# Performance work log

Measured on AMD Instinct MI355X. Metric: run time of the kernel, lower is better.

Reference implementation:

```python
import jax, jax.numpy as jnp
import numpy as np

TOPK = 4          # config.top_prob_values
NBINS = 32        # config.max_num_bins -> bins per corner = NBINS+1 = 33
HID = 64          # config.lqe_hidden_dim
B, L = 64, 4096


def setup_inputs() -> dict:
    key = jax.random.key(0)
    k1, k2, k3, k4 = jax.random.split(key, 4)
    in_dim = 4 * (TOPK + 1)  # 20
    scores = jax.random.normal(k1, (B, L, 1), dtype=jnp.float32)
    pred_corners = jax.random.normal(k2, (B, L, 4 * (NBINS + 1)), dtype=jnp.float32)
    # Deimv2MLP (DFineMLP) with num_layers=2: Linear(20,64) -> relu -> Linear(64,1)
    w1 = jax.random.normal(k3, (in_dim, HID), dtype=jnp.float32) / np.sqrt(in_dim)
    b1 = jnp.zeros((HID,), dtype=jnp.float32)
    w2 = jax.random.normal(k4, (HID, 1), dtype=jnp.float32) / np.sqrt(HID)
    b2 = jnp.zeros((1,), dtype=jnp.float32)
    return {"scores": scores, "pred_corners": pred_corners,
            "w1": w1, "b1": b1, "w2": w2, "b2": b2}


def reference(scores, pred_corners, w1, b1, w2, b2):
    b, l, _ = pred_corners.shape
    # softmax over bins per corner: (B, L, 4, NBINS+1)
    prob = jax.nn.softmax(pred_corners.reshape(b, l, 4, NBINS + 1), axis=-1)
    prob_topk, _ = jax.lax.top_k(prob, TOPK)                     # (B, L, 4, TOPK)
    stat = jnp.concatenate([prob_topk,
                            prob_topk.mean(axis=-1, keepdims=True)], axis=-1)
    stat = stat.reshape(b, l, 4 * (TOPK + 1))                    # (B, L, 20)
    h = jax.nn.relu(stat @ w1 + b1)                              # (B, L, 64)
    quality_score = h @ w2 + b2                                  # (B, L, 1)
    return scores + quality_score
```

## Files before the change

### kernel.cpp

```cpp
#include <hip/hip_runtime.h>


#define THREADS 256
#define ROWS 64

typedef float f32x4 __attribute__((ext_vector_type(4), aligned(16)));

__device__ __forceinline__ void sort4d(float& a, float& b, float& c, float& d) {
    float t;
    t = fmaxf(a, b); b = fminf(a, b); a = t;
    t = fmaxf(c, d); d = fminf(c, d); c = t;
    t = fmaxf(a, c); c = fminf(a, c); a = t;
    t = fmaxf(b, d); d = fminf(b, d); b = t;
    t = fmaxf(b, c); c = fminf(b, c); b = t;
}
__device__ __forceinline__ void ins4(float& a, float& b, float& c, float& d,
                                     float x) {
    float t;
    t = fmaxf(a, x); x = fminf(a, x); a = t;
    t = fmaxf(b, x); x = fminf(b, x); b = t;
    t = fmaxf(c, x); x = fminf(c, x); c = t;
    d = fmaxf(d, x);
}
__device__ __forceinline__ void merge4(float& a0, float& a1, float& a2,
                                       float& a3, float b0, float b1,
                                       float b2, float b3) {
    a0 = fmaxf(a0, b3);
    a1 = fmaxf(a1, b2);
    a2 = fmaxf(a2, b1);
    a3 = fmaxf(a3, b0);
    sort4d(a0, a1, a2, a3);
}

__global__ __launch_bounds__(THREADS, 4)
void lqe_kernel(const float* __restrict__ scores,
                const float* __restrict__ pc,
                const float* __restrict__ w1,
                const float* __restrict__ b1,
                const float* __restrict__ w2,
                const float* __restrict__ b2,
                float* __restrict__ out)
{
    __shared__ float sm_stage[ROWS * 132];
    __shared__ float sm_stat[ROWS * 21];

    const int t = threadIdx.x;
    const long long rowBase = (long long)blockIdx.x * ROWS;

    {
        const f32x4* __restrict__ src = (const f32x4*)(pc + rowBase * 132);
        f32x4* dst = (f32x4*)sm_stage;
        #pragma unroll
        for (int i = 0; i < 8; ++i) dst[t + i * 256] = src[t + i * 256];
        if (t < 64) dst[2048 + t] = src[2048 + t];
    }
    __syncthreads();

    {
        const float* v = sm_stage + t * 33;
        float x[33];
        #pragma unroll
        for (int k = 0; k < 33; ++k) x[k] = v[k];

        float a0 = x[0],  a1 = x[1],  a2 = x[2],  a3 = x[3];
        float c0 = x[8],  c1 = x[9],  c2 = x[10], c3 = x[11];
        float d0 = x[16], d1 = x[17], d2 = x[18], d3 = x[19];
        float e0 = x[24], e1 = x[25], e2 = x[26], e3 = x[27];
        sort4d(a0, a1, a2, a3);
        sort4d(c0, c1, c2, c3);
        sort4d(d0, d1, d2, d3);
        sort4d(e0, e1, e2, e3);
        #pragma unroll
        for (int k = 0; k < 4; ++k) {
            ins4(a0, a1, a2, a3, x[4 + k]);
            ins4(c0, c1, c2, c3, x[12 + k]);
            ins4(d0, d1, d2, d3, x[20 + k]);
            ins4(e0, e1, e2, e3, x[28 + k]);
        }
        ins4(e0, e1, e2, e3, x[32]);
        merge4(a0, a1, a2, a3, c0, c1, c2, c3);
        merge4(d0, d1, d2, d3, e0, e1, e2, e3);
        merge4(a0, a1, a2, a3, d0, d1, d2, d3);
        const float t0 = a0, t1 = a1, t2 = a2, t3 = a3;

        float sa = 0.f, sb = 0.f, sc = 0.f, sd = 0.f;
        #pragma unroll
        for (int k = 0; k < 32; k += 4) {
            sa += __expf(x[k + 0] - t0);
            sb += __expf(x[k + 1] - t0);
            sc += __expf(x[k + 2] - t0);
            sd += __expf(x[k + 3] - t0);
        }
        sa += __expf(x[32] - t0);
        const float inv = 1.0f / ((sa + sb) + (sc + sd));
        const float p0 = inv;
        const float p1 = __expf(t1 - t0) * inv;
        const float p2 = __expf(t2 - t0) * inv;
        const float p3 = __expf(t3 - t0) * inv;
        const float pm = 0.25f * (p0 + p1 + p2 + p3);

        float* sd_ = sm_stat + (t >> 2) * 21 + (t & 3) * 5;
        sd_[0] = p0; sd_[1] = p1; sd_[2] = p2; sd_[3] = p3; sd_[4] = pm;
    }
    __syncthreads();

    {
        const int l  = t & 63;
        const int wv = __builtin_amdgcn_readfirstlane(t >> 6);
        const float* __restrict__ w1s = w1 + wv * 16;
        const float* __restrict__ w2s = w2 + wv * 16;
        const float* __restrict__ b1s = b1 + wv * 16;

        float st[20];
        #pragma unroll
        for (int k = 0; k < 20; ++k) st[k] = sm_stat[l * 21 + k];

        float h[16];
        #pragma unroll
        for (int j = 0; j < 16; ++j) h[j] = b1s[j];
        #pragma unroll
        for (int k = 0; k < 20; ++k) {
            #pragma unroll
            for (int j = 0; j < 16; ++j)
                h[j] = fmaf(st[k], w1s[k * 64 + j], h[j]);
        }
        float acc0 = 0.f, acc1 = 0.f, acc2 = 0.f, acc3 = 0.f;
        #pragma unroll
        for (int j = 0; j < 16; j += 4) {
            acc0 = fmaf(fmaxf(h[j + 0], 0.f), w2s[j + 0], acc0);
            acc1 = fmaf(fmaxf(h[j + 1], 0.f), w2s[j + 1], acc1);
            acc2 = fmaf(fmaxf(h[j + 2], 0.f), w2s[j + 2], acc2);
            acc3 = fmaf(fmaxf(h[j + 3], 0.f), w2s[j + 3], acc3);
        }
        sm_stage[wv * 64 + l] = (acc0 + acc1) + (acc2 + acc3);
    }
    __syncthreads();

    if (t < 64) {
        const float r = (sm_stage[t] + sm_stage[64 + t]) +
                        (sm_stage[128 + t] + sm_stage[192 + t]);
        out[rowBase + t] = scores[rowBase + t] + r + b2[0];
    }
}

extern "C" void kernel_launch(void* const* d_in, const int* in_sizes, int n_in,
                              void* d_out, int out_size, void* d_ws, size_t ws_size,
                              hipStream_t stream) {
    const float* scores = (const float*)d_in[0];
    const float* pc     = (const float*)d_in[1];
    const float* w1     = (const float*)d_in[2];
    const float* b1     = (const float*)d_in[3];
    const float* w2     = (const float*)d_in[4];
    const float* b2     = (const float*)d_in[5];
    float* out = (float*)d_out;

    const int rows = out_size;
    const int blocks = rows / ROWS;
    lqe_kernel<<<blocks, THREADS, 0, stream>>>(scores, pc, w1, b1, w2, b2, out);
}
```

Before: 32.66 us.

## Double-buffer row groups with async global-to-LDS loads across persistent blocks

Each block now handles eight groups of 64 rows instead of one. Two LDS buffers alternate: the next group is prefetched with global_load_lds (direct global-to-LDS DMA) while the current group's softmax, top-k and MLP run. The aim is to hide load latency behind compute and cut per-block launch and staging overhead. The cost is about double the LDS per block and launch bounds lowered to 2 blocks per CU, so fewer loads are in flight per CU, which may hurt a kernel that is limited by memory bandwidth.

```diff
diff --git a/kernel.cpp b/kernel.cpp
--- a/kernel.cpp
+++ b/kernel.cpp
@@ -2,9 +2,18 @@
 
 
 #define THREADS 256
-#define ROWS 64
+#define GROUPS 8
+#define GROUP_ROWS 64
 
 typedef float f32x4 __attribute__((ext_vector_type(4), aligned(16)));
+
+#define BAR_LGKM() asm volatile("s_waitcnt lgkmcnt(0)\n\ts_barrier" ::: "memory")
+
+__device__ __forceinline__ void gll16(const float* g, float* l) {
+    __builtin_amdgcn_global_load_lds(
+        (const __attribute__((address_space(1))) void*)g,
+        (__attribute__((address_space(3))) void*)l, 16, 0, 0);
+}
 
 __device__ __forceinline__ void sort4d(float& a, float& b, float& c, float& d) {
     float t;
@@ -32,7 +41,7 @@
     sort4d(a0, a1, a2, a3);
 }
 
-__global__ __launch_bounds__(THREADS, 4)
+__global__ __launch_bounds__(THREADS, 2)
 void lqe_kernel(const float* __restrict__ scores,
                 const float* __restrict__ pc,
                 const float* __restrict__ w1,
@@ -41,23 +50,28 @@
                 const float* __restrict__ b2,
                 float* __restrict__ out)
 {
-    __shared__ float sm_stage[ROWS * 132];
-    __shared__ float sm_stat[ROWS * 21];
+    __shared__ float smA[GROUP_ROWS * 132];
+    __shared__ float smB[GROUP_ROWS * 132];
+    __shared__ float smStat[GROUP_ROWS * 21];
 
     const int t = threadIdx.x;
-    const long long rowBase = (long long)blockIdx.x * ROWS;
-
-    {
-        const f32x4* __restrict__ src = (const f32x4*)(pc + rowBase * 132);
-        f32x4* dst = (f32x4*)sm_stage;
-        #pragma unroll
-        for (int i = 0; i < 8; ++i) dst[t + i * 256] = src[t + i * 256];
-        if (t < 64) dst[2048 + t] = src[2048 + t];
-    }
-    __syncthreads();
-
-    {
-        const float* v = sm_stage + t * 33;
+    const int l = t & 63;
+    const long long blockRow0 = (long long)blockIdx.x * (GROUPS * GROUP_ROWS);
+    const float b2v = b2[0];
+
+    auto stage_async = [&](int g, float* buf) {
+        const float* src = pc + (blockRow0 + (long long)g * GROUP_ROWS) * 132;
+        const int wvOff = __builtin_amdgcn_readfirstlane(t >> 6) * 64;
+        #pragma unroll
+        for (int i = 0; i < 8; ++i)
+            gll16(src + (size_t)(i * 256 + wvOff + l) * 4,
+                  buf + (size_t)(i * 256 + wvOff) * 4);
+        if (t < 64)
+            gll16(src + (size_t)(2048 + l) * 4, buf + (size_t)2048 * 4);
+    };
+
+    auto corner = [&](const float* buf) {
+        const float* v = buf + t * 33;
         float x[33];
         #pragma unroll
         for (int k = 0; k < 33; ++k) x[k] = v[k];
@@ -99,13 +113,11 @@
         const float p3 = __expf(t3 - t0) * inv;
         const float pm = 0.25f * (p0 + p1 + p2 + p3);
 
-        float* sd_ = sm_stat + (t >> 2) * 21 + (t & 3) * 5;
+        float* sd_ = smStat + (t >> 2) * 21 + (t & 3) * 5;
         sd_[0] = p0; sd_[1] = p1; sd_[2] = p2; sd_[3] = p3; sd_[4] = pm;
-    }
-    __syncthreads();
-
-    {
-        const int l  = t & 63;
+    };
+
+    auto mlp = [&](float* buf) {
         const int wv = __builtin_amdgcn_readfirstlane(t >> 6);
         const float* __restrict__ w1s = w1 + wv * 16;
         const float* __restrict__ w2s = w2 + wv * 16;
@@ -113,7 +125,7 @@
 
         float st[20];
         #pragma unroll
-        for (int k = 0; k < 20; ++k) st[k] = sm_stat[l * 21 + k];
+        for (int k = 0; k < 20; ++k) st[k] = smStat[l * 21 + k];
 
         float h[16];
         #pragma unroll
@@ -132,14 +144,42 @@
             acc2 = fmaf(fmaxf(h[j + 2], 0.f), w2s[j + 2], acc2);
             acc3 = fmaf(fmaxf(h[j + 3], 0.f), w2s[j + 3], acc3);
         }
-        sm_stage[wv * 64 + l] = (acc0 + acc1) + (acc2 + acc3);
-    }
+        buf[wv * 64 + l] = (acc0 + acc1) + (acc2 + acc3);
+    };
+
+    stage_async(0, smA);
     __syncthreads();
 
-    if (t < 64) {
-        const float r = (sm_stage[t] + sm_stage[64 + t]) +
-                        (sm_stage[128 + t] + sm_stage[192 + t]);
-        out[rowBase + t] = scores[rowBase + t] + r + b2[0];
+    #pragma unroll 1
+    for (int gp = 0; gp < GROUPS; gp += 2) {
+        {
+            float sc0 = 0.f;
+            if (t < 64) sc0 = scores[blockRow0 + (long long)gp * 64 + t];
+            if (gp + 1 < GROUPS) stage_async(gp + 1, smB);
+            corner(smA);
+            BAR_LGKM();
+            mlp(smA);
+            BAR_LGKM();
+            if (t < 64)
+                out[blockRow0 + (long long)gp * 64 + t] =
+                    sc0 + (smA[t] + smA[64 + t]) + (smA[128 + t] + smA[192 + t]) + b2v;
+            asm volatile("s_waitcnt vmcnt(0)" ::: "memory");
+            __syncthreads();
+        }
+        {
+            float sc1 = 0.f;
+            if (t < 64) sc1 = scores[blockRow0 + (long long)(gp + 1) * 64 + t];
+            if (gp + 2 < GROUPS) stage_async(gp + 2, smA);
+            corner(smB);
+            BAR_LGKM();
+            mlp(smB);
+            BAR_LGKM();
+            if (t < 64)
+                out[blockRow0 + (long long)(gp + 1) * 64 + t] =
+                    sc1 + (smB[t] + smB[64 + t]) + (smB[128 + t] + smB[192 + t]) + b2v;
+            asm volatile("s_waitcnt vmcnt(0)" ::: "memory");
+            __syncthreads();
+        }
     }
 }
 
@@ -155,6 +195,6 @@
     float* out = (float*)d_out;
 
     const int rows = out_size;
-    const int blocks = rows / ROWS;
+    const int blocks = rows / (GROUPS * GROUP_ROWS);
     lqe_kernel<<<blocks, THREADS, 0, stream>>>(scores, pc, w1, b1, w2, b2, out);
 }
```

Result: slower. 37.89 us (+16.0%).

## Process two row tiles per block with register-prefetched second tile

Applied to the files above, without the earlier changes.

Each block now handles 128 rows instead of 64. Both 64-row tiles of pred_corners (and the scores) are loaded into registers up front, so the second tile's global load overlaps the first tile's softmax/top-k and MLP. The plain __syncthreads are replaced with an inline s_waitcnt lgkmcnt(0) + s_barrier, which avoids waiting on outstanding global loads at each barrier. The cost is roughly 64 extra VGPRs for the buffered tile and half as many blocks, which may lower occupancy for a kernel that is mostly bandwidth-bound.

```diff
diff --git a/kernel.cpp b/kernel.cpp
--- a/kernel.cpp
+++ b/kernel.cpp
@@ -2,9 +2,10 @@
 
 
 #define THREADS 256
-#define ROWS 64
 
 typedef float f32x4 __attribute__((ext_vector_type(4), aligned(16)));
+
+#define BAR_LGKM() asm volatile("s_waitcnt lgkmcnt(0)\n\ts_barrier" ::: "memory")
 
 __device__ __forceinline__ void sort4d(float& a, float& b, float& c, float& d) {
     float t;
@@ -30,6 +31,89 @@
     a2 = fmaxf(a2, b1);
     a3 = fmaxf(a3, b0);
     sort4d(a0, a1, a2, a3);
+}
+
+__device__ __forceinline__ void corner_phase(const float* __restrict__ stage,
+                                             float* __restrict__ stat, int t) {
+    const float* v = stage + t * 33;
+    float x[33];
+    #pragma unroll
+    for (int k = 0; k < 33; ++k) x[k] = v[k];
+
+    float a0 = x[0],  a1 = x[1],  a2 = x[2],  a3 = x[3];
+    float c0 = x[8],  c1 = x[9],  c2 = x[10], c3 = x[11];
+    float d0 = x[16], d1 = x[17], d2 = x[18], d3 = x[19];
+    float e0 = x[24], e1 = x[25], e2 = x[26], e3 = x[27];
+    sort4d(a0, a1, a2, a3);
+    sort4d(c0, c1, c2, c3);
+    sort4d(d0, d1, d2, d3);
+    sort4d(e0, e1, e2, e3);
+    #pragma unroll
+    for (int k = 0; k < 4; ++k) {
+        ins4(a0, a1, a2, a3, x[4 + k]);
+        ins4(c0, c1, c2, c3, x[12 + k]);
+        ins4(d0, d1, d2, d3, x[20 + k]);
+        ins4(e0, e1, e2, e3, x[28 + k]);
+    }
+    ins4(e0, e1, e2, e3, x[32]);
+    merge4(a0, a1, a2, a3, c0, c1, c2, c3);
+    merge4(d0, d1, d2, d3, e0, e1, e2, e3);
+    merge4(a0, a1, a2, a3, d0, d1, d2, d3);
+    const float t0 = a0, t1 = a1, t2 = a2, t3 = a3;
+
+    float sa = 0.f, sb = 0.f, sc = 0.f, sd = 0.f;
+    #pragma unroll
+    for (int k = 0; k < 32; k += 4) {
+        sa += __expf(x[k + 0] - t0);
+        sb += __expf(x[k + 1] - t0);
+        sc += __expf(x[k + 2] - t0);
+        sd += __expf(x[k + 3] - t0);
+    }
+    sa += __expf(x[32] - t0);
+    const float inv = 1.0f / ((sa + sb) + (sc + sd));
+    const float p0 = inv;
+    const float p1 = __expf(t1 - t0) * inv;
+    const float p2 = __expf(t2 - t0) * inv;
+    const float p3 = __expf(t3 - t0) * inv;
+    const float pm = 0.25f * (p0 + p1 + p2 + p3);
+
+    float* sd_ = stat + (t >> 2) * 21 + (t & 3) * 5;
+    sd_[0] = p0; sd_[1] = p1; sd_[2] = p2; sd_[3] = p3; sd_[4] = pm;
+}
+
+__device__ __forceinline__ void mlp_phase(const float* __restrict__ stat,
+                                          float* __restrict__ part, int t,
+                                          const float* __restrict__ w1,
+                                          const float* __restrict__ b1,
+                                          const float* __restrict__ w2) {
+    const int l  = t & 63;
+    const int wv = __builtin_amdgcn_readfirstlane(t >> 6);
+    const float* __restrict__ w1s = w1 + wv * 16;
+    const float* __restrict__ w2s = w2 + wv * 16;
+    const float* __restrict__ b1s = b1 + wv * 16;
+
+    float st[20];
+    #pragma unroll
+    for (int k = 0; k < 20; ++k) st[k] = stat[l * 21 + k];
+
+    float h[16];
+    #pragma unroll
+    for (int j = 0; j < 16; ++j) h[j] = b1s[j];
+    #pragma unroll
+    for (int k = 0; k < 20; ++k) {
+        #pragma unroll
+        for (int j = 0; j < 16; ++j)
+            h[j] = fmaf(st[k], w1s[k * 64 + j], h[j]);
+    }
+    float acc0 = 0.f, acc1 = 0.f, acc2 = 0.f, acc3 = 0.f;
+    #pragma unroll
+    for (int j = 0; j < 16; j += 4) {
+        acc0 = fmaf(fmaxf(h[j + 0], 0.f), w2s[j + 0], acc0);
+        acc1 = fmaf(fmaxf(h[j + 1], 0.f), w2s[j + 1], acc1);
+        acc2 = fmaf(fmaxf(h[j + 2], 0.f), w2s[j + 2], acc2);
+        acc3 = fmaf(fmaxf(h[j + 3], 0.f), w2s[j + 3], acc3);
+    }
+    part[wv * 64 + l] = (acc0 + acc1) + (acc2 + acc3);
 }
 
 __global__ __launch_bounds__(THREADS, 4)
@@ -41,106 +125,64 @@
                 const float* __restrict__ b2,
                 float* __restrict__ out)
 {
-    __shared__ float sm_stage[ROWS * 132];
-    __shared__ float sm_stat[ROWS * 21];
+    __shared__ float smStage[64 * 132];
+    __shared__ float smStat[64 * 21];
+    __shared__ float smPart[256];
 
     const int t = threadIdx.x;
-    const long long rowBase = (long long)blockIdx.x * ROWS;
+    const long long rowBase = (long long)blockIdx.x * 128;
+    const float b2v = b2[0];
+
+    float sc0 = 0.f, sc1 = 0.f;
+    if (t < 64) {
+        sc0 = scores[rowBase + t];
+        sc1 = scores[rowBase + 64 + t];
+    }
+
+    const f32x4* __restrict__ s0 = (const f32x4*)(pc + rowBase * 132);
+    const f32x4* __restrict__ s1 = (const f32x4*)(pc + (rowBase + 64) * 132);
+    f32x4 ra[8], rb[8], taA = {0,0,0,0}, tbB = {0,0,0,0};
+    #pragma unroll
+    for (int i = 0; i < 8; ++i) ra[i] = s0[t + i * 256];
+    if (t < 64) taA = s0[2048 + t];
+    #pragma unroll
+    for (int i = 0; i < 8; ++i) rb[i] = s1[t + i * 256];
+    if (t < 64) tbB = s1[2048 + t];
+    __builtin_amdgcn_sched_barrier(0);
 
     {
-        const f32x4* __restrict__ src = (const f32x4*)(pc + rowBase * 132);
-        f32x4* dst = (f32x4*)sm_stage;
+        f32x4* dst = (f32x4*)smStage;
         #pragma unroll
-        for (int i = 0; i < 8; ++i) dst[t + i * 256] = src[t + i * 256];
-        if (t < 64) dst[2048 + t] = src[2048 + t];
-    }
-    __syncthreads();
+        for (int i = 0; i < 8; ++i) dst[t + i * 256] = ra[i];
+        if (t < 64) dst[2048 + t] = taA;
+    }
+    BAR_LGKM();
+
+    corner_phase(smStage, smStat, t);
+    BAR_LGKM();
+    mlp_phase(smStat, smPart, t, w1, b1, w2);
+    BAR_LGKM();
+    if (t < 64)
+        out[rowBase + t] =
+            sc0 + (smPart[t] + smPart[64 + t]) +
+                  (smPart[128 + t] + smPart[192 + t]) + b2v;
 
     {
-        const float* v = sm_stage + t * 33;
-        float x[33];
+        f32x4* dst = (f32x4*)smStage;
         #pragma unroll
-        for (int k = 0; k < 33; ++k) x[k] = v[k];
-
-        float a0 = x[0],  a1 = x[1],  a2 = x[2],  a3 = x[3];
-        float c0 = x[8],  c1 = x[9],  c2 = x[10], c3 = x[11];
-        float d0 = x[16], d1 = x[17], d2 = x[18], d3 = x[19];
-        float e0 = x[24], e1 = x[25], e2 = x[26], e3 = x[27];
-        sort4d(a0, a1, a2, a3);
-        sort4d(c0, c1, c2, c3);
-        sort4d(d0, d1, d2, d3);
-        sort4d(e0, e1, e2, e3);
-        #pragma unroll
-        for (int k = 0; k < 4; ++k) {
-            ins4(a0, a1, a2, a3, x[4 + k]);
-            ins4(c0, c1, c2, c3, x[12 + k]);
-            ins4(d0, d1, d2, d3, x[20 + k]);
-            ins4(e0, e1, e2, e3, x[28 + k]);
-        }
-        ins4(e0, e1, e2, e3, x[32]);
-        merge4(a0, a1, a2, a3, c0, c1, c2, c3);
-        merge4(d0, d1, d2, d3, e0, e1, e2, e3);
-        merge4(a0, a1, a2, a3, d0, d1, d2, d3);
-        const float t0 = a0, t1 = a1, t2 = a2, t3 = a3;
-
-        float sa = 0.f, sb = 0.f, sc = 0.f, sd = 0.f;
-        #pragma unroll
-        for (int k = 0; k < 32; k += 4) {
-            sa += __expf(x[k + 0] - t0);
-            sb += __expf(x[k + 1] - t0);
-            sc += __expf(x[k + 2] - t0);
-            sd += __expf(x[k + 3] - t0);
-        }
-        sa += __expf(x[32] - t0);
-        const float inv = 1.0f / ((sa + sb) + (sc + sd));
-        const float p0 = inv;
-        const float p1 = __expf(t1 - t0) * inv;
-        const float p2 = __expf(t2 - t0) * inv;
-        const float p3 = __expf(t3 - t0) * inv;
-        const float pm = 0.25f * (p0 + p1 + p2 + p3);
-
-        float* sd_ = sm_stat + (t >> 2) * 21 + (t & 3) * 5;
-        sd_[0] = p0; sd_[1] = p1; sd_[2] = p2; sd_[3] = p3; sd_[4] = pm;
-    }
-    __syncthreads();
-
-    {
-        const int l  = t & 63;
-        const int wv = __builtin_amdgcn_readfirstlane(t >> 6);
-        const float* __restrict__ w1s = w1 + wv * 16;
-        const float* __restrict__ w2s = w2 + wv * 16;
-        const float* __restrict__ b1s = b1 + wv * 16;
-
-        float st[20];
-        #pragma unroll
-        for (int k = 0; k < 20; ++k) st[k] = sm_stat[l * 21 + k];
-
-        float h[16];
-        #pragma unroll
-        for (int j = 0; j < 16; ++j) h[j] = b1s[j];
-        #pragma unroll
-        for (int k = 0; k < 20; ++k) {
-            #pragma unroll
-            for (int j = 0; j < 16; ++j)
-                h[j] = fmaf(st[k], w1s[k * 64 + j], h[j]);
-        }
-        float acc0 = 0.f, acc1 = 0.f, acc2 = 0.f, acc3 = 0.f;
-        #pragma unroll
-        for (int j = 0; j < 16; j += 4) {
-            acc0 = fmaf(fmaxf(h[j + 0], 0.f), w2s[j + 0], acc0);
-            acc1 = fmaf(fmaxf(h[j + 1], 0.f), w2s[j + 1], acc1);
-            acc2 = fmaf(fmaxf(h[j + 2], 0.f), w2s[j + 2], acc2);
-            acc3 = fmaf(fmaxf(h[j + 3], 0.f), w2s[j + 3], acc3);
-        }
-        sm_stage[wv * 64 + l] = (acc0 + acc1) + (acc2 + acc3);
-    }
-    __syncthreads();
-
-    if (t < 64) {
-        const float r = (sm_stage[t] + sm_stage[64 + t]) +
-                        (sm_stage[128 + t] + sm_stage[192 + t]);
-        out[rowBase + t] = scores[rowBase + t] + r + b2[0];
-    }
+        for (int i = 0; i < 8; ++i) dst[t + i * 256] = rb[i];
+        if (t < 64) dst[2048 + t] = tbB;
+    }
+    BAR_LGKM();
+
+    corner_phase(smStage, smStat, t);
+    BAR_LGKM();
+    mlp_phase(smStat, smPart, t, w1, b1, w2);
+    BAR_LGKM();
+    if (t < 64)
+        out[rowBase + 64 + t] =
+            sc1 + (smPart[t] + smPart[64 + t]) +
+                  (smPart[128 + t] + smPart[192 + t]) + b2v;
 }
 
 extern "C" void kernel_launch(void* const* d_in, const int* in_sizes, int n_in,
@@ -155,6 +197,6 @@
     float* out = (float*)d_out;
 
     const int rows = out_size;
-    const int blocks = rows / ROWS;
+    const int blocks = rows / 128;
     lqe_kernel<<<blocks, THREADS, 0, stream>>>(scores, pc, w1, b1, w2, b2, out);
 }
```

Result: slower. 37.50 us (+14.8%).
